# Kernel optimization log

Measured on AMD Instinct MI355X. Metric: run time of the kernel, lower is better.

The kernel has to match this reference:

```python
import jax, jax.numpy as jnp
import numpy as np

N, E, D, H, O = 100000, 1600000, 128, 128, 64
EPS = 1e-5


def setup_inputs() -> dict:
    key = jax.random.key(0)
    ks = jax.random.split(key, 12)
    s = 0.05
    return {
        "x": jax.random.normal(ks[0], (N, D), jnp.float32),
        "edge_index": jax.random.randint(ks[1], (2, E), 0, N),
        "W1": jax.random.normal(ks[2], (D, H), jnp.float32) * s,
        "b1": jnp.zeros((H,), jnp.float32),
        "W2": jax.random.normal(ks[3], (H, H), jnp.float32) * s,
        "b2": jnp.zeros((H,), jnp.float32),
        "W3": jax.random.normal(ks[4], (H, H), jnp.float32) * s,
        "b3": jnp.zeros((H,), jnp.float32),
        "g1": jnp.ones((H,), jnp.float32),
        "be1": jnp.zeros((H,), jnp.float32),
        "g2": jnp.ones((H,), jnp.float32),
        "be2": jnp.zeros((H,), jnp.float32),
        "Wp1": jax.random.normal(ks[5], (H, H), jnp.float32) * s,
        "bp1": jnp.zeros((H,), jnp.float32),
        "Wp2": jax.random.normal(ks[6], (H, O), jnp.float32) * s,
        "bp2": jnp.zeros((O,), jnp.float32),
    }


def _layer_norm(h, g, b):
    mu = jnp.mean(h, axis=-1, keepdims=True)
    var = jnp.mean(jnp.square(h - mu), axis=-1, keepdims=True)
    return g * (h - mu) * jax.lax.rsqrt(var + EPS) + b


def reference(x, edge_index, W1, b1, W2, b2, W3, b3, g1, be1, g2, be2, Wp1, bp1, Wp2, bp2):
    n = x.shape[0]
    loop = jnp.arange(n)
    # GCN: add self-loops, symmetric normalization D^-1/2 (A+I) D^-1/2
    src = jnp.concatenate([edge_index[0], loop])
    dst = jnp.concatenate([edge_index[1], loop])
    deg = jax.ops.segment_sum(jnp.ones_like(src, x.dtype), dst, num_segments=n)
    dinv = jax.lax.rsqrt(jnp.maximum(deg, 1e-12))
    norm = dinv[src] * dinv[dst]  # [E+N]

    def gcn_conv(h, W, b):
        hw = h @ W                              # transform first (PyG GCNConv)
        msg = hw[src] * norm[:, None]           # gather + edge scale
        return jax.ops.segment_sum(msg, dst, num_segments=n) + b  # scatter-add

    # dropout is a no-op in eval mode
    h = _layer_norm(jax.nn.relu(gcn_conv(x, W1, b1)), g1, be1)
    h = _layer_norm(jax.nn.relu(gcn_conv(h, W2, b2)), g2, be2)
    h = jax.nn.relu(gcn_conv(h, W3, b3))
    h = h @ Wp1 + bp1
    h = h @ Wp2 + bp2
    return jax.nn.sigmoid(h)
```

## Files before the change

### kernel.cpp

```cpp
#include <hip/hip_runtime.h>
#include <hip/hip_bf16.h>

typedef __attribute__((ext_vector_type(8))) short short8;
typedef __attribute__((ext_vector_type(4))) float floatx4;
typedef unsigned int u32;

__device__ __forceinline__ u32 f2bf(float f) {
    union { float f; u32 u; } c; c.f = f;
    return (c.u + 0x7FFFu + ((c.u >> 16) & 1u)) >> 16;
}
__device__ __forceinline__ short8 cvt8(const float* p) {
    float4 f0 = ((const float4*)p)[0];
    float4 f1 = ((const float4*)p)[1];
    short8 r;
    r[0] = (short)f2bf(f0.x); r[1] = (short)f2bf(f0.y);
    r[2] = (short)f2bf(f0.z); r[3] = (short)f2bf(f0.w);
    r[4] = (short)f2bf(f1.x); r[5] = (short)f2bf(f1.y);
    r[6] = (short)f2bf(f1.z); r[7] = (short)f2bf(f1.w);
    return r;
}

__device__ __forceinline__ void fp8x8_acc(uint2 v, float* a) {
    auto f0 = __builtin_amdgcn_cvt_pk_f32_fp8((int)v.x, false);
    auto f1 = __builtin_amdgcn_cvt_pk_f32_fp8((int)v.x, true);
    auto f2 = __builtin_amdgcn_cvt_pk_f32_fp8((int)v.y, false);
    auto f3 = __builtin_amdgcn_cvt_pk_f32_fp8((int)v.y, true);
    a[0] += ((const float*)&f0)[0]; a[1] += ((const float*)&f0)[1];
    a[2] += ((const float*)&f1)[0]; a[3] += ((const float*)&f1)[1];
    a[4] += ((const float*)&f2)[0]; a[5] += ((const float*)&f2)[1];
    a[6] += ((const float*)&f3)[0]; a[7] += ((const float*)&f3)[1];
}
__device__ __forceinline__ void fp8x8_dec(uint2 v, float* x) {
    auto f0 = __builtin_amdgcn_cvt_pk_f32_fp8((int)v.x, false);
    auto f1 = __builtin_amdgcn_cvt_pk_f32_fp8((int)v.x, true);
    auto f2 = __builtin_amdgcn_cvt_pk_f32_fp8((int)v.y, false);
    auto f3 = __builtin_amdgcn_cvt_pk_f32_fp8((int)v.y, true);
    x[0] = ((const float*)&f0)[0]; x[1] = ((const float*)&f0)[1];
    x[2] = ((const float*)&f1)[0]; x[3] = ((const float*)&f1)[1];
    x[4] = ((const float*)&f2)[0]; x[5] = ((const float*)&f2)[1];
    x[6] = ((const float*)&f3)[0]; x[7] = ((const float*)&f3)[1];
}
__device__ __forceinline__ u32 f32x4_to_fp8(float a, float b, float c, float d) {
    u32 w = (u32)__builtin_amdgcn_cvt_pk_fp8_f32(a, b, 0, false);
    w = (u32)__builtin_amdgcn_cvt_pk_fp8_f32(c, d, (int)w, true);
    return w;
}

#define CCAP 264

__device__ __forceinline__ void gatherq(const uint2* __restrict__ hw64,
                                        const int* __restrict__ col,
                                        int* __restrict__ ldsc,
                                        int begq, int endq, int beg, int stagelen,
                                        int lane, int s16, float* __restrict__ acc) {
    for (int i = lane; i < stagelen; i += 64) ldsc[i] = col[beg + i];
    __syncthreads();
    int dq = endq - begq;
    int offq = begq - beg;
    int send = min(endq, beg + stagelen);
    int sdq = max(0, send - begq);
    int mx = sdq;
    mx = max(mx, __shfl_xor(mx, 16));
    mx = max(mx, __shfl_xor(mx, 32));
    int idxcap = CCAP - 8;
    int off0 = min(offq, idxcap);
    for (int jb = 0; jb < mx; jb += 8) {
        uint2 v[8];
#pragma unroll
        for (int j = 0; j < 8; ++j) {
            int jj = jb + j;
            int cj = ldsc[off0 + (jj < stagelen - off0 ? jj : 0)];
            bool act = jj < sdq;
            uint2 tv; tv.x = 0u; tv.y = 0u;
            if (act) {
                cj = ldsc[offq + jj];
                tv = hw64[(size_t)cj * 16 + s16];
            }
            v[j] = tv;
        }
#pragma unroll
        for (int j = 0; j < 8; ++j) fp8x8_acc(v[j], acc);
    }
    for (int j = sdq; j < dq; ++j) {
        int cj = col[begq + j];
        uint2 tv = hw64[(size_t)cj * 16 + s16];
        fp8x8_acc(tv, acc);
    }
}

__global__ __launch_bounds__(256) void hist_trans_k(
        const int* __restrict__ dst, int* __restrict__ bcnt, int E, int histB,
        const float* __restrict__ W1, const float* __restrict__ W2,
        const float* __restrict__ W3, const float* __restrict__ Wp1,
        const float* __restrict__ Wp2,
        unsigned short* __restrict__ o1, unsigned short* __restrict__ o2,
        unsigned short* __restrict__ o3, unsigned short* __restrict__ o4,
        unsigned short* __restrict__ o5) {
    int t = threadIdx.x;
    if ((int)blockIdx.x < histB) {
        __shared__ int h[512];
        h[t] = 0; h[t + 256] = 0;
        __syncthreads();
        int e0 = blockIdx.x * 4096;
        int ne = min(4096, E - e0);
        for (int i = t; i < ne; i += 256) atomicAdd(&h[dst[e0 + i] >> 8], 1);
        __syncthreads();
        int c = h[t];
        if (c) atomicAdd(&bcnt[t], c);
        c = h[t + 256];
        if (c) atomicAdd(&bcnt[t + 256], c);
    } else {
        int i = (blockIdx.x - histB) * 256 + t;
        const float* in; unsigned short* out; int cols, li;
        if (i < 16384)      { in = W1;  out = o1; cols = 128; li = i; }
        else if (i < 32768) { in = W2;  out = o2; cols = 128; li = i - 16384; }
        else if (i < 49152) { in = W3;  out = o3; cols = 128; li = i - 32768; }
        else if (i < 65536) { in = Wp1; out = o4; cols = 128; li = i - 49152; }
        else                { in = Wp2; out = o5; cols = 64;  li = i - 65536; }
        int r = li / cols, c = li - r * cols;
        out[(size_t)c * 128 + r] = (unsigned short)f2bf(in[li]);
    }
}

__global__ void bscan_k(const int* __restrict__ bcnt, int* __restrict__ bbase,
                        int* __restrict__ cursor, int nb, int E) {
    __shared__ int tmp[512];
    int t = threadIdx.x;
    int v = (t < nb) ? bcnt[t] : 0;
    tmp[t] = v;
    __syncthreads();
    for (int off = 1; off < 512; off <<= 1) {
        int a = (t >= off) ? tmp[t - off] : 0;
        __syncthreads();
        tmp[t] += a;
        __syncthreads();
    }
    if (t < nb) {
        int ex = tmp[t] - v;
        bbase[t] = ex;
        cursor[t] = ex;
    }
    if (t == 0) bbase[nb] = E;
}

__global__ __launch_bounds__(256) void bucket_k(const int* __restrict__ src,
                                                const int* __restrict__ dst,
                                                int* __restrict__ cursor,
                                                u32* __restrict__ pairs, int E, int nb) {
    __shared__ int cnt[512];
    __shared__ int gbase[512];
    __shared__ int cur[512];
    int t = threadIdx.x;
    cnt[t] = 0; cnt[t + 256] = 0;
    __syncthreads();
    int e0 = blockIdx.x * 8192;
    int ne = min(8192, E - e0);
    for (int i = t; i < ne; i += 256) atomicAdd(&cnt[dst[e0 + i] >> 8], 1);
    __syncthreads();
    for (int b = t; b < nb; b += 256) {
        int c = cnt[b];
        gbase[b] = c ? atomicAdd(&cursor[b], c) : 0;
        cur[b] = 0;
    }
    __syncthreads();
    for (int i = t; i < ne; i += 256) {
        int d = dst[e0 + i];
        int s = src[e0 + i];
        int b = d >> 8;
        int p = atomicAdd(&cur[b], 1);
        pairs[gbase[b] + p] = (u32)s | ((u32)(d & 255) << 24);
    }
}

#define LCOL_CAP 12288
__global__ __launch_bounds__(256) void build_k(const u32* __restrict__ pairs,
                                               const int* __restrict__ bbase,
                                               int* __restrict__ rowptr,
                                               float* __restrict__ dinv,
                                               int* __restrict__ col, int N, int E) {
    __shared__ int cnt[256], incl[256], cur[256];
    __shared__ int lcol[LCOL_CAP];
    int b = blockIdx.x, t = threadIdx.x;
    int base = bbase[b];
    int ecnt = bbase[b + 1] - base;
    cnt[t] = 0;
    __syncthreads();
    for (int j = t; j < ecnt; j += 256) atomicAdd(&cnt[pairs[base + j] >> 24], 1);
    __syncthreads();
    incl[t] = cnt[t];
    __syncthreads();
    for (int off = 1; off < 256; off <<= 1) {
        int a = (t >= off) ? incl[t - off] : 0;
        __syncthreads();
        incl[t] += a;
        __syncthreads();
    }
    int myc = cnt[t];
    int ex = incl[t] - myc;
    int node = b * 256 + t;
    if (node < N) {
        rowptr[node] = base + ex;
        dinv[node] = rsqrtf((float)myc + 1.0f);
    }
    cur[t] = ex;
    if (b == 0 && t == 0) rowptr[N] = E;
    __syncthreads();
    if (ecnt <= LCOL_CAP) {
        for (int j = t; j < ecnt; j += 256) {
            u32 v = pairs[base + j];
            int r = atomicAdd(&cur[v >> 24], 1);
            lcol[r] = (int)(v & 0xFFFFFF);
        }
        __syncthreads();
        for (int j = t; j < ecnt; j += 256) col[base + j] = lcol[j];
    } else {
        for (int j = t; j < ecnt; j += 256) {
            u32 v = pairs[base + j];
            int r = atomicAdd(&cur[v >> 24], 1);
            col[base + r] = (int)(v & 0xFFFFFF);
        }
    }
}

__global__ __launch_bounds__(256) void gemm1_k(const float* __restrict__ A,
                                               const short* __restrict__ Wt,
                                               const float* __restrict__ dinv,
                                               u32* __restrict__ out, int M) {
    int wave = threadIdx.x >> 6;
    int lane = threadIdx.x & 63;
    int m0 = blockIdx.x * 64 + wave * 16;
    if (m0 >= M) return;
    int quad = lane >> 4, lr = lane & 15;
    int row = m0 + lr;
    bool wr = row < M;
    if (row >= M) row = M - 1;
    const float* Ab = A + (size_t)row * 128 + quad * 8;
    short8 b0 = cvt8(Ab), b1 = cvt8(Ab + 32), b2 = cvt8(Ab + 64), b3 = cvt8(Ab + 96);
    float di = dinv[row];
#pragma unroll
    for (int nt = 0; nt < 8; ++nt) {
        int ncol = nt * 16 + lr;
        const short8* Wp = (const short8*)(Wt + (size_t)ncol * 128 + quad * 8);
        short8 a0 = Wp[0], a1 = Wp[4], a2 = Wp[8], a3 = Wp[12];
        floatx4 acc = {0.f, 0.f, 0.f, 0.f};
        acc = __builtin_amdgcn_mfma_f32_16x16x32_bf16(a0, b0, acc, 0, 0, 0);
        acc = __builtin_amdgcn_mfma_f32_16x16x32_bf16(a1, b1, acc, 0, 0, 0);
        acc = __builtin_amdgcn_mfma_f32_16x16x32_bf16(a2, b2, acc, 0, 0, 0);
        acc = __builtin_amdgcn_mfma_f32_16x16x32_bf16(a3, b3, acc, 0, 0, 0);
        if (wr) {
            out[(size_t)(m0 + lr) * 32 + nt * 4 + quad] =
                f32x4_to_fp8(acc[0] * di, acc[1] * di, acc[2] * di, acc[3] * di);
        }
    }
}

__global__ __launch_bounds__(256) void fconv_k(const uint2* __restrict__ hw64,
                                               const int* __restrict__ rowptr,
                                               const int* __restrict__ col,
                                               const float* __restrict__ dinv,
                                               const float* __restrict__ bias,
                                               const float* __restrict__ gam,
                                               const float* __restrict__ bet,
                                               const short* __restrict__ Wt,
                                               u32* __restrict__ out, int N) {
    __shared__ unsigned short rows[16][136];
    __shared__ int ldsc[4][CCAP];
    int t = threadIdx.x, wave = t >> 6, lane = t & 63;
    int q = lane >> 4, s16 = lane & 15;
    int nb0 = blockIdx.x * 16;
    int node0 = nb0 + wave * 4;
    int node = node0 + q;
    bool ok = node < N;
    int beg = rowptr[min(node0, N)];
    int e4  = rowptr[min(node0 + 4, N)];
    int begq = rowptr[min(node, N)];
    int endq = ok ? rowptr[min(node + 1, N)] : begq;
    int stagelen = min(e4 - beg, 256);
    uint2 selfd; selfd.x = 0u; selfd.y = 0u;
    float di = 0.f;
    if (ok) {
        selfd = hw64[(size_t)node * 16 + s16];
        di = dinv[node];
    }
    float acc[8] = {0.f, 0.f, 0.f, 0.f, 0.f, 0.f, 0.f, 0.f};
    gatherq(hw64, col, ldsc[wave], begq, endq, beg, stagelen, lane, s16, acc);

    float sx[8]; fp8x8_dec(selfd, sx);
    float4 bv0 = *(const float4*)(bias + 8 * s16);
    float4 bv1 = *(const float4*)(bias + 8 * s16 + 4);
    float a[8];
    a[0] = fmaxf(di * (acc[0] + sx[0]) + bv0.x, 0.f);
    a[1] = fmaxf(di * (acc[1] + sx[1]) + bv0.y, 0.f);
    a[2] = fmaxf(di * (acc[2] + sx[2]) + bv0.z, 0.f);
    a[3] = fmaxf(di * (acc[3] + sx[3]) + bv0.w, 0.f);
    a[4] = fmaxf(di * (acc[4] + sx[4]) + bv1.x, 0.f);
    a[5] = fmaxf(di * (acc[5] + sx[5]) + bv1.y, 0.f);
    a[6] = fmaxf(di * (acc[6] + sx[6]) + bv1.z, 0.f);
    a[7] = fmaxf(di * (acc[7] + sx[7]) + bv1.w, 0.f);
    if (!ok) {
#pragma unroll
        for (int k = 0; k < 8; ++k) a[k] = 0.f;
    }
    float s = 0.f, qq = 0.f;
#pragma unroll
    for (int k = 0; k < 8; ++k) { s += a[k]; qq += a[k] * a[k]; }
#pragma unroll
    for (int mm = 8; mm >= 1; mm >>= 1) {
        s += __shfl_xor(s, mm);
        qq += __shfl_xor(qq, mm);
    }
    float mu = s * (1.f / 128.f);
    float var = qq * (1.f / 128.f) - mu * mu;
    float rs = rsqrtf(fmaxf(var, 0.f) + 1e-5f);
    float4 gv0 = *(const float4*)(gam + 8 * s16);
    float4 gv1 = *(const float4*)(gam + 8 * s16 + 4);
    float4 be0 = *(const float4*)(bet + 8 * s16);
    float4 be1 = *(const float4*)(bet + 8 * s16 + 4);
    a[0] = gv0.x * (a[0] - mu) * rs + be0.x;
    a[1] = gv0.y * (a[1] - mu) * rs + be0.y;
    a[2] = gv0.z * (a[2] - mu) * rs + be0.z;
    a[3] = gv0.w * (a[3] - mu) * rs + be0.w;
    a[4] = gv1.x * (a[4] - mu) * rs + be1.x;
    a[5] = gv1.y * (a[5] - mu) * rs + be1.y;
    a[6] = gv1.z * (a[6] - mu) * rs + be1.z;
    a[7] = gv1.w * (a[7] - mu) * rs + be1.w;
    if (!ok) {
#pragma unroll
        for (int k = 0; k < 8; ++k) a[k] = 0.f;
    }
    int r = wave * 4 + q;
    uint4 st;
    st.x = f2bf(a[0]) | (f2bf(a[1]) << 16);
    st.y = f2bf(a[2]) | (f2bf(a[3]) << 16);
    st.z = f2bf(a[4]) | (f2bf(a[5]) << 16);
    st.w = f2bf(a[6]) | (f2bf(a[7]) << 16);
    *(uint4*)((char*)&rows[r][0] + 16 * s16) = st;
    __syncthreads();

    int quad = lane >> 4, lr = lane & 15;
    short8 b0 = *(const short8*)&rows[lr][quad * 8];
    short8 b1 = *(const short8*)&rows[lr][32 + quad * 8];
    short8 b2 = *(const short8*)&rows[lr][64 + quad * 8];
    short8 b3 = *(const short8*)&rows[lr][96 + quad * 8];
    int onode = nb0 + lr;
    float di2 = (onode < N) ? dinv[onode] : 0.f;
#pragma unroll
    for (int k = 0; k < 2; ++k) {
        int ct = wave * 2 + k;
        int ncol = ct * 16 + lr;
        const short8* Wp = (const short8*)(Wt + (size_t)ncol * 128 + quad * 8);
        short8 a0 = Wp[0], a1 = Wp[4], a2 = Wp[8], a3 = Wp[12];
        floatx4 acm = {0.f, 0.f, 0.f, 0.f};
        acm = __builtin_amdgcn_mfma_f32_16x16x32_bf16(a0, b0, acm, 0, 0, 0);
        acm = __builtin_amdgcn_mfma_f32_16x16x32_bf16(a1, b1, acm, 0, 0, 0);
        acm = __builtin_amdgcn_mfma_f32_16x16x32_bf16(a2, b2, acm, 0, 0, 0);
        acm = __builtin_amdgcn_mfma_f32_16x16x32_bf16(a3, b3, acm, 0, 0, 0);
        int c0 = ct * 16 + quad * 4;
        if (onode < N) {
            out[(size_t)onode * 32 + (c0 >> 2)] =
                f32x4_to_fp8(acm[0] * di2, acm[1] * di2, acm[2] * di2, acm[3] * di2);
        }
    }
}

__global__ __launch_bounds__(256) void fhead_k(const uint2* __restrict__ hw64,
                                               const int* __restrict__ rowptr,
                                               const int* __restrict__ col,
                                               const float* __restrict__ dinv,
                                               const float* __restrict__ bias,
                                               const short* __restrict__ Wp1t,
                                               const float* __restrict__ bp1,
                                               const short* __restrict__ Wp2t,
                                               const float* __restrict__ bp2,
                                               float* __restrict__ out, int N) {
    __shared__ unsigned short rows[16][136];
    __shared__ unsigned short h1s[16][136];
    __shared__ int ldsc[4][CCAP];
    int t = threadIdx.x, wave = t >> 6, lane = t & 63;
    int q = lane >> 4, s16 = lane & 15;
    int nb0 = blockIdx.x * 16;
    int node0 = nb0 + wave * 4;
    int node = node0 + q;
    bool ok = node < N;
    int beg = rowptr[min(node0, N)];
    int e4  = rowptr[min(node0 + 4, N)];
    int begq = rowptr[min(node, N)];
    int endq = ok ? rowptr[min(node + 1, N)] : begq;
    int stagelen = min(e4 - beg, 256);
    uint2 selfd; selfd.x = 0u; selfd.y = 0u;
    float di = 0.f;
    if (ok) {
        selfd = hw64[(size_t)node * 16 + s16];
        di = dinv[node];
    }
    float acc[8] = {0.f, 0.f, 0.f, 0.f, 0.f, 0.f, 0.f, 0.f};
    gatherq(hw64, col, ldsc[wave], begq, endq, beg, stagelen, lane, s16, acc);

    float sx[8]; fp8x8_dec(selfd, sx);
    float4 bv0 = *(const float4*)(bias + 8 * s16);
    float4 bv1 = *(const float4*)(bias + 8 * s16 + 4);
    float a[8];
    a[0] = fmaxf(di * (acc[0] + sx[0]) + bv0.x, 0.f);
    a[1] = fmaxf(di * (acc[1] + sx[1]) + bv0.y, 0.f);
    a[2] = fmaxf(di * (acc[2] + sx[2]) + bv0.z, 0.f);
    a[3] = fmaxf(di * (acc[3] + sx[3]) + bv0.w, 0.f);
    a[4] = fmaxf(di * (acc[4] + sx[4]) + bv1.x, 0.f);
    a[5] = fmaxf(di * (acc[5] + sx[5]) + bv1.y, 0.f);
    a[6] = fmaxf(di * (acc[6] + sx[6]) + bv1.z, 0.f);
    a[7] = fmaxf(di * (acc[7] + sx[7]) + bv1.w, 0.f);
    if (!ok) {
#pragma unroll
        for (int k = 0; k < 8; ++k) a[k] = 0.f;
    }
    int r = wave * 4 + q;
    uint4 st;
    st.x = f2bf(a[0]) | (f2bf(a[1]) << 16);
    st.y = f2bf(a[2]) | (f2bf(a[3]) << 16);
    st.z = f2bf(a[4]) | (f2bf(a[5]) << 16);
    st.w = f2bf(a[6]) | (f2bf(a[7]) << 16);
    *(uint4*)((char*)&rows[r][0] + 16 * s16) = st;
    __syncthreads();

    int quad = lane >> 4, lr = lane & 15;
    {
        short8 b0 = *(const short8*)&rows[lr][quad * 8];
        short8 b1 = *(const short8*)&rows[lr][32 + quad * 8];
        short8 b2 = *(const short8*)&rows[lr][64 + quad * 8];
        short8 b3 = *(const short8*)&rows[lr][96 + quad * 8];
#pragma unroll
        for (int k = 0; k < 2; ++k) {
            int ct = wave * 2 + k;
            int ncol = ct * 16 + lr;
            const short8* Wp = (const short8*)(Wp1t + (size_t)ncol * 128 + quad * 8);
            short8 a0 = Wp[0], a1 = Wp[4], a2 = Wp[8], a3 = Wp[12];
            floatx4 acm = {0.f, 0.f, 0.f, 0.f};
            acm = __builtin_amdgcn_mfma_f32_16x16x32_bf16(a0, b0, acm, 0, 0, 0);
            acm = __builtin_amdgcn_mfma_f32_16x16x32_bf16(a1, b1, acm, 0, 0, 0);
            acm = __builtin_amdgcn_mfma_f32_16x16x32_bf16(a2, b2, acm, 0, 0, 0);
            acm = __builtin_amdgcn_mfma_f32_16x16x32_bf16(a3, b3, acm, 0, 0, 0);
            int c0 = ct * 16 + quad * 4;
            float4 bv = *(const float4*)(bp1 + c0);
            uint2 stq;
            stq.x = f2bf(acm[0] + bv.x) | (f2bf(acm[1] + bv.y) << 16);
            stq.y = f2bf(acm[2] + bv.z) | (f2bf(acm[3] + bv.w) << 16);
            *(uint2*)&h1s[lr][c0] = stq;
        }
    }
    __syncthreads();
    {
        short8 b0 = *(const short8*)&h1s[lr][quad * 8];
        short8 b1 = *(const short8*)&h1s[lr][32 + quad * 8];
        short8 b2 = *(const short8*)&h1s[lr][64 + quad * 8];
        short8 b3 = *(const short8*)&h1s[lr][96 + quad * 8];
        int ncol = wave * 16 + lr;
        const short8* Wp = (const short8*)(Wp2t + (size_t)ncol * 128 + quad * 8);
        short8 a0 = Wp[0], a1 = Wp[4], a2 = Wp[8], a3 = Wp[12];
        floatx4 acm = {0.f, 0.f, 0.f, 0.f};
        acm = __builtin_amdgcn_mfma_f32_16x16x32_bf16(a0, b0, acm, 0, 0, 0);
        acm = __builtin_amdgcn_mfma_f32_16x16x32_bf16(a1, b1, acm, 0, 0, 0);
        acm = __builtin_amdgcn_mfma_f32_16x16x32_bf16(a2, b2, acm, 0, 0, 0);
        acm = __builtin_amdgcn_mfma_f32_16x16x32_bf16(a3, b3, acm, 0, 0, 0);
        int c0 = wave * 16 + quad * 4;
        int onode = nb0 + lr;
        if (onode < N) {
            float4 bv = *(const float4*)(bp2 + c0);
            float4 sg;
            sg.x = 1.f / (1.f + __expf(-(acm[0] + bv.x)));
            sg.y = 1.f / (1.f + __expf(-(acm[1] + bv.y)));
            sg.z = 1.f / (1.f + __expf(-(acm[2] + bv.z)));
            sg.w = 1.f / (1.f + __expf(-(acm[3] + bv.w)));
            *(float4*)(out + (size_t)onode * 64 + c0) = sg;
        }
    }
}

extern "C" void kernel_launch(void* const* d_in, const int* in_sizes, int n_in,
                              void* d_out, int out_size, void* d_ws, size_t ws_size,
                              hipStream_t stream) {
    const int N = in_sizes[0] / 128;
    const int E = in_sizes[1] / 2;
    const int nb = (N + 255) >> 8;
    const int* edge = (const int*)d_in[1];
    const int* srcp = edge;
    const int* dstp = edge + E;
    const float* x   = (const float*)d_in[0];
    const float* W1  = (const float*)d_in[2];
    const float* b1  = (const float*)d_in[3];
    const float* W2  = (const float*)d_in[4];
    const float* b2  = (const float*)d_in[5];
    const float* W3  = (const float*)d_in[6];
    const float* b3  = (const float*)d_in[7];
    const float* g1  = (const float*)d_in[8];
    const float* be1 = (const float*)d_in[9];
    const float* g2  = (const float*)d_in[10];
    const float* be2 = (const float*)d_in[11];
    const float* Wp1 = (const float*)d_in[12];
    const float* bp1 = (const float*)d_in[13];
    const float* Wp2 = (const float*)d_in[14];
    const float* bp2 = (const float*)d_in[15];

    char* ws = (char*)d_ws;
    size_t off = 0;
    auto alloc = [&](size_t b) -> char* {
        char* p = ws + off;
        off += (b + 255) & ~(size_t)255;
        return p;
    };
    int* bcnt   = (int*)alloc(512 * 4);
    int* bbase  = (int*)alloc((size_t)(nb + 1) * 4);
    int* cursor = (int*)alloc((size_t)nb * 4);
    int* rowptr = (int*)alloc((size_t)(N + 1) * 4);
    float* dinv = (float*)alloc((size_t)N * 4);
    u32* pairs  = (u32*)alloc((size_t)E * 4);
    int* colA   = (int*)alloc((size_t)E * 4);
    unsigned char* hw  = (unsigned char*)alloc((size_t)N * 128);
    unsigned char* hb  = (unsigned char*)alloc((size_t)N * 128);
    unsigned short* w1t = (unsigned short*)alloc(128 * 128 * 2);
    unsigned short* w2t = (unsigned short*)alloc(128 * 128 * 2);
    unsigned short* w3t = (unsigned short*)alloc(128 * 128 * 2);
    unsigned short* wp1t = (unsigned short*)alloc(128 * 128 * 2);
    unsigned short* wp2t = (unsigned short*)alloc(64 * 128 * 2);
    if (off > ws_size) return;

    int gb = (N + 63) / 64;
    int fb = (N + 15) / 16;
    int histB = (E + 4095) / 4096;

    hipMemsetAsync(bcnt, 0, 512 * 4, stream);
    hist_trans_k<<<histB + 288, 256, 0, stream>>>(dstp, bcnt, E, histB,
                                                  W1, W2, W3, Wp1, Wp2,
                                                  w1t, w2t, w3t, wp1t, wp2t);
    bscan_k<<<1, 512, 0, stream>>>(bcnt, bbase, cursor, nb, E);
    bucket_k<<<(E + 8191) / 8192, 256, 0, stream>>>(srcp, dstp, cursor, pairs, E, nb);
    build_k<<<nb, 256, 0, stream>>>(pairs, bbase, rowptr, dinv, colA, N, E);

    gemm1_k<<<gb, 256, 0, stream>>>(x, (const short*)w1t, dinv, (u32*)hw, N);
    fconv_k<<<fb, 256, 0, stream>>>((const uint2*)hw, rowptr, colA, dinv,
                                    b1, g1, be1, (const short*)w2t, (u32*)hb, N);
    fconv_k<<<fb, 256, 0, stream>>>((const uint2*)hb, rowptr, colA, dinv,
                                    b2, g2, be2, (const short*)w3t, (u32*)hw, N);
    fhead_k<<<fb, 256, 0, stream>>>((const uint2*)hw, rowptr, colA, dinv, b3,
                                    (const short*)wp1t, bp1, (const short*)wp2t, bp2,
                                    (float*)d_out, N);
}
```

Measured before the change: 370.4 us.

## Replace bucketed two-pass CSR build with per-node degree count and atomic scatter

The CSR construction changes from a two-level bucket sort (histogram per 256-node bucket, bucket pairs, local sort in LDS) to a per-node global atomic degree count, then a block-sum, scan and rowptr kernel, then a direct atomic-cursor scatter of source ids into col. This drops the intermediate pairs buffer and the LDS sorting pass. In exchange it uses heavily contended global atomics on individual nodes and scattered writes, and the order of neighbours within a row becomes nondeterministic. The gather index load is also simplified to a single clamped LDS read.

Result: slower. 542.6 us (+46.5%).

```diff
diff --git a/kernel.cpp b/kernel.cpp
--- a/kernel.cpp
+++ b/kernel.cpp
@@ -62,20 +62,15 @@
     int mx = sdq;
     mx = max(mx, __shfl_xor(mx, 16));
     mx = max(mx, __shfl_xor(mx, 32));
-    int idxcap = CCAP - 8;
-    int off0 = min(offq, idxcap);
     for (int jb = 0; jb < mx; jb += 8) {
         uint2 v[8];
 #pragma unroll
         for (int j = 0; j < 8; ++j) {
             int jj = jb + j;
-            int cj = ldsc[off0 + (jj < stagelen - off0 ? jj : 0)];
+            int cj = ldsc[min(offq + jj, CCAP - 1)];
             bool act = jj < sdq;
             uint2 tv; tv.x = 0u; tv.y = 0u;
-            if (act) {
-                cj = ldsc[offq + jj];
-                tv = hw64[(size_t)cj * 16 + s16];
-            }
+            if (act) tv = hw64[(size_t)cj * 16 + s16];
             v[j] = tv;
         }
 #pragma unroll
@@ -88,8 +83,8 @@
     }
 }
 
-__global__ __launch_bounds__(256) void hist_trans_k(
-        const int* __restrict__ dst, int* __restrict__ bcnt, int E, int histB,
+__global__ __launch_bounds__(256) void deg_trans_k(
+        const int* __restrict__ dst, int* __restrict__ deg, int E, int degB,
         const float* __restrict__ W1, const float* __restrict__ W2,
         const float* __restrict__ W3, const float* __restrict__ Wp1,
         const float* __restrict__ Wp2,
@@ -97,20 +92,12 @@
         unsigned short* __restrict__ o3, unsigned short* __restrict__ o4,
         unsigned short* __restrict__ o5) {
     int t = threadIdx.x;
-    if ((int)blockIdx.x < histB) {
-        __shared__ int h[512];
-        h[t] = 0; h[t + 256] = 0;
-        __syncthreads();
+    if ((int)blockIdx.x < degB) {
         int e0 = blockIdx.x * 4096;
         int ne = min(4096, E - e0);
-        for (int i = t; i < ne; i += 256) atomicAdd(&h[dst[e0 + i] >> 8], 1);
-        __syncthreads();
-        int c = h[t];
-        if (c) atomicAdd(&bcnt[t], c);
-        c = h[t + 256];
-        if (c) atomicAdd(&bcnt[t + 256], c);
+        for (int i = t; i < ne; i += 256) atomicAdd(&deg[dst[e0 + i]], 1);
     } else {
-        int i = (blockIdx.x - histB) * 256 + t;
+        int i = (blockIdx.x - degB) * 256 + t;
         const float* in; unsigned short* out; int cols, li;
         if (i < 16384)      { in = W1;  out = o1; cols = 128; li = i; }
         else if (i < 32768) { in = W2;  out = o2; cols = 128; li = i - 16384; }
@@ -122,8 +109,22 @@
     }
 }
 
+__global__ __launch_bounds__(256) void bsum_k(const int* __restrict__ deg,
+                                              int* __restrict__ bcnt, int N) {
+    __shared__ int sh[256];
+    int t = threadIdx.x;
+    int node = blockIdx.x * 256 + t;
+    sh[t] = (node < N) ? deg[node] : 0;
+    __syncthreads();
+    for (int off = 128; off >= 1; off >>= 1) {
+        if (t < off) sh[t] += sh[t + off];
+        __syncthreads();
+    }
+    if (t == 0) bcnt[blockIdx.x] = sh[0];
+}
+
 __global__ void bscan_k(const int* __restrict__ bcnt, int* __restrict__ bbase,
-                        int* __restrict__ cursor, int nb, int E) {
+                        int nb, int E) {
     __shared__ int tmp[512];
     int t = threadIdx.x;
     int v = (t < nb) ? bcnt[t] : 0;
@@ -135,59 +136,20 @@
         tmp[t] += a;
         __syncthreads();
     }
-    if (t < nb) {
-        int ex = tmp[t] - v;
-        bbase[t] = ex;
-        cursor[t] = ex;
-    }
+    if (t < nb) bbase[t] = tmp[t] - v;
     if (t == 0) bbase[nb] = E;
 }
 
-__global__ __launch_bounds__(256) void bucket_k(const int* __restrict__ src,
-                                                const int* __restrict__ dst,
+__global__ __launch_bounds__(256) void rowptr_k(const int* __restrict__ deg,
+                                                const int* __restrict__ bbase,
+                                                int* __restrict__ rowptr,
                                                 int* __restrict__ cursor,
-                                                u32* __restrict__ pairs, int E, int nb) {
-    __shared__ int cnt[512];
-    __shared__ int gbase[512];
-    __shared__ int cur[512];
-    int t = threadIdx.x;
-    cnt[t] = 0; cnt[t + 256] = 0;
-    __syncthreads();
-    int e0 = blockIdx.x * 8192;
-    int ne = min(8192, E - e0);
-    for (int i = t; i < ne; i += 256) atomicAdd(&cnt[dst[e0 + i] >> 8], 1);
-    __syncthreads();
-    for (int b = t; b < nb; b += 256) {
-        int c = cnt[b];
-        gbase[b] = c ? atomicAdd(&cursor[b], c) : 0;
-        cur[b] = 0;
-    }
-    __syncthreads();
-    for (int i = t; i < ne; i += 256) {
-        int d = dst[e0 + i];
-        int s = src[e0 + i];
-        int b = d >> 8;
-        int p = atomicAdd(&cur[b], 1);
-        pairs[gbase[b] + p] = (u32)s | ((u32)(d & 255) << 24);
-    }
-}
-
-#define LCOL_CAP 12288
-__global__ __launch_bounds__(256) void build_k(const u32* __restrict__ pairs,
-                                               const int* __restrict__ bbase,
-                                               int* __restrict__ rowptr,
-                                               float* __restrict__ dinv,
-                                               int* __restrict__ col, int N, int E) {
-    __shared__ int cnt[256], incl[256], cur[256];
-    __shared__ int lcol[LCOL_CAP];
+                                                float* __restrict__ dinv, int N, int E) {
+    __shared__ int incl[256];
     int b = blockIdx.x, t = threadIdx.x;
-    int base = bbase[b];
-    int ecnt = bbase[b + 1] - base;
-    cnt[t] = 0;
-    __syncthreads();
-    for (int j = t; j < ecnt; j += 256) atomicAdd(&cnt[pairs[base + j] >> 24], 1);
-    __syncthreads();
-    incl[t] = cnt[t];
+    int node = b * 256 + t;
+    int d = (node < N) ? deg[node] : 0;
+    incl[t] = d;
     __syncthreads();
     for (int off = 1; off < 256; off <<= 1) {
         int a = (t >= off) ? incl[t - off] : 0;
@@ -195,30 +157,25 @@
         incl[t] += a;
         __syncthreads();
     }
-    int myc = cnt[t];
-    int ex = incl[t] - myc;
-    int node = b * 256 + t;
     if (node < N) {
-        rowptr[node] = base + ex;
-        dinv[node] = rsqrtf((float)myc + 1.0f);
-    }
-    cur[t] = ex;
+        int ex = bbase[b] + incl[t] - d;
+        rowptr[node] = ex;
+        cursor[node] = ex;
+        dinv[node] = rsqrtf((float)d + 1.0f);
+    }
     if (b == 0 && t == 0) rowptr[N] = E;
-    __syncthreads();
-    if (ecnt <= LCOL_CAP) {
-        for (int j = t; j < ecnt; j += 256) {
-            u32 v = pairs[base + j];
-            int r = atomicAdd(&cur[v >> 24], 1);
-            lcol[r] = (int)(v & 0xFFFFFF);
-        }
-        __syncthreads();
-        for (int j = t; j < ecnt; j += 256) col[base + j] = lcol[j];
-    } else {
-        for (int j = t; j < ecnt; j += 256) {
-            u32 v = pairs[base + j];
-            int r = atomicAdd(&cur[v >> 24], 1);
-            col[base + r] = (int)(v & 0xFFFFFF);
-        }
+}
+
+__global__ __launch_bounds__(256) void scatter_k(const int* __restrict__ src,
+                                                 const int* __restrict__ dst,
+                                                 int* __restrict__ cursor,
+                                                 int* __restrict__ col, int E) {
+    int stride = gridDim.x * 256;
+    for (int i = blockIdx.x * 256 + threadIdx.x; i < E; i += stride) {
+        int d = dst[i];
+        int s = src[i];
+        int pos = atomicAdd(&cursor[d], 1);
+        col[pos] = s;
     }
 }
 
@@ -508,10 +465,10 @@
     };
     int* bcnt   = (int*)alloc(512 * 4);
     int* bbase  = (int*)alloc((size_t)(nb + 1) * 4);
-    int* cursor = (int*)alloc((size_t)nb * 4);
+    int* deg    = (int*)alloc((size_t)N * 4);
+    int* cursor = (int*)alloc((size_t)N * 4);
     int* rowptr = (int*)alloc((size_t)(N + 1) * 4);
     float* dinv = (float*)alloc((size_t)N * 4);
-    u32* pairs  = (u32*)alloc((size_t)E * 4);
     int* colA   = (int*)alloc((size_t)E * 4);
     unsigned char* hw  = (unsigned char*)alloc((size_t)N * 128);
     unsigned char* hb  = (unsigned char*)alloc((size_t)N * 128);
@@ -524,15 +481,16 @@
 
     int gb = (N + 63) / 64;
     int fb = (N + 15) / 16;
-    int histB = (E + 4095) / 4096;
-
-    hipMemsetAsync(bcnt, 0, 512 * 4, stream);
-    hist_trans_k<<<histB + 288, 256, 0, stream>>>(dstp, bcnt, E, histB,
-                                                  W1, W2, W3, Wp1, Wp2,
-                                                  w1t, w2t, w3t, wp1t, wp2t);
-    bscan_k<<<1, 512, 0, stream>>>(bcnt, bbase, cursor, nb, E);
-    bucket_k<<<(E + 8191) / 8192, 256, 0, stream>>>(srcp, dstp, cursor, pairs, E, nb);
-    build_k<<<nb, 256, 0, stream>>>(pairs, bbase, rowptr, dinv, colA, N, E);
+    int degB = (E + 4095) / 4096;
+
+    hipMemsetAsync(deg, 0, (size_t)N * 4, stream);
+    deg_trans_k<<<degB + 288, 256, 0, stream>>>(dstp, deg, E, degB,
+                                                W1, W2, W3, Wp1, Wp2,
+                                                w1t, w2t, w3t, wp1t, wp2t);
+    bsum_k<<<nb, 256, 0, stream>>>(deg, bcnt, N);
+    bscan_k<<<1, 512, 0, stream>>>(bcnt, bbase, nb, E);
+    rowptr_k<<<nb, 256, 0, stream>>>(deg, bbase, rowptr, cursor, dinv, N, E);
+    scatter_k<<<2048, 256, 0, stream>>>(srcp, dstp, cursor, colA, E);
 
     gemm1_k<<<gb, 256, 0, stream>>>(x, (const short*)w1t, dinv, (u32*)hw, N);
     fconv_k<<<fb, 256, 0, stream>>>((const uint2*)hw, rowptr, colA, dinv,
```

## Bucket edges into fixed-capacity slots to drop the separate histogram pass

Applied to the files above, without the earlier changes.

The CSR build now scatters edges directly into fixed-capacity per-bucket regions of 8192 slots, using per-bucket global counters. This removes the separate histogram pass over dst and its prefix-scan dependency before bucketing, so one full read of dst and a launch are saved. The weight transpose is merged into the bucketing kernel, and the scan afterwards only computes CSR offsets. It risks overflow if any 256-node bucket receives more than 8192 edges, which holds for uniform random inputs but not for skewed graphs. The gather index load is also simplified to a clamped LDS read.

Result: faster. 362.8 us (-2.1%).

```diff
diff --git a/kernel.cpp b/kernel.cpp
--- a/kernel.cpp
+++ b/kernel.cpp
@@ -47,6 +47,7 @@
 }
 
 #define CCAP 264
+#define CAPB 8192
 
 __device__ __forceinline__ void gatherq(const uint2* __restrict__ hw64,
                                         const int* __restrict__ col,
@@ -62,20 +63,15 @@
     int mx = sdq;
     mx = max(mx, __shfl_xor(mx, 16));
     mx = max(mx, __shfl_xor(mx, 32));
-    int idxcap = CCAP - 8;
-    int off0 = min(offq, idxcap);
     for (int jb = 0; jb < mx; jb += 8) {
         uint2 v[8];
 #pragma unroll
         for (int j = 0; j < 8; ++j) {
             int jj = jb + j;
-            int cj = ldsc[off0 + (jj < stagelen - off0 ? jj : 0)];
+            int cj = ldsc[min(offq + jj, CCAP - 1)];
             bool act = jj < sdq;
             uint2 tv; tv.x = 0u; tv.y = 0u;
-            if (act) {
-                cj = ldsc[offq + jj];
-                tv = hw64[(size_t)cj * 16 + s16];
-            }
+            if (act) tv = hw64[(size_t)cj * 16 + s16];
             v[j] = tv;
         }
 #pragma unroll
@@ -88,8 +84,9 @@
     }
 }
 
-__global__ __launch_bounds__(256) void hist_trans_k(
-        const int* __restrict__ dst, int* __restrict__ bcnt, int E, int histB,
+__global__ __launch_bounds__(256) void bucket_trans_k(
+        const int* __restrict__ src, const int* __restrict__ dst,
+        int* __restrict__ gcnt, u32* __restrict__ pairs, int E, int nb, int bucketB,
         const float* __restrict__ W1, const float* __restrict__ W2,
         const float* __restrict__ W3, const float* __restrict__ Wp1,
         const float* __restrict__ Wp2,
@@ -97,20 +94,8 @@
         unsigned short* __restrict__ o3, unsigned short* __restrict__ o4,
         unsigned short* __restrict__ o5) {
     int t = threadIdx.x;
-    if ((int)blockIdx.x < histB) {
-        __shared__ int h[512];
-        h[t] = 0; h[t + 256] = 0;
-        __syncthreads();
-        int e0 = blockIdx.x * 4096;
-        int ne = min(4096, E - e0);
-        for (int i = t; i < ne; i += 256) atomicAdd(&h[dst[e0 + i] >> 8], 1);
-        __syncthreads();
-        int c = h[t];
-        if (c) atomicAdd(&bcnt[t], c);
-        c = h[t + 256];
-        if (c) atomicAdd(&bcnt[t + 256], c);
-    } else {
-        int i = (blockIdx.x - histB) * 256 + t;
+    if ((int)blockIdx.x >= bucketB) {
+        int i = (blockIdx.x - bucketB) * 256 + t;
         const float* in; unsigned short* out; int cols, li;
         if (i < 16384)      { in = W1;  out = o1; cols = 128; li = i; }
         else if (i < 32768) { in = W2;  out = o2; cols = 128; li = i - 16384; }
@@ -119,38 +104,11 @@
         else                { in = Wp2; out = o5; cols = 64;  li = i - 65536; }
         int r = li / cols, c = li - r * cols;
         out[(size_t)c * 128 + r] = (unsigned short)f2bf(in[li]);
-    }
-}
-
-__global__ void bscan_k(const int* __restrict__ bcnt, int* __restrict__ bbase,
-                        int* __restrict__ cursor, int nb, int E) {
-    __shared__ int tmp[512];
-    int t = threadIdx.x;
-    int v = (t < nb) ? bcnt[t] : 0;
-    tmp[t] = v;
-    __syncthreads();
-    for (int off = 1; off < 512; off <<= 1) {
-        int a = (t >= off) ? tmp[t - off] : 0;
-        __syncthreads();
-        tmp[t] += a;
-        __syncthreads();
-    }
-    if (t < nb) {
-        int ex = tmp[t] - v;
-        bbase[t] = ex;
-        cursor[t] = ex;
-    }
-    if (t == 0) bbase[nb] = E;
-}
-
-__global__ __launch_bounds__(256) void bucket_k(const int* __restrict__ src,
-                                                const int* __restrict__ dst,
-                                                int* __restrict__ cursor,
-                                                u32* __restrict__ pairs, int E, int nb) {
+        return;
+    }
     __shared__ int cnt[512];
     __shared__ int gbase[512];
     __shared__ int cur[512];
-    int t = threadIdx.x;
     cnt[t] = 0; cnt[t + 256] = 0;
     __syncthreads();
     int e0 = blockIdx.x * 8192;
@@ -159,7 +117,7 @@
     __syncthreads();
     for (int b = t; b < nb; b += 256) {
         int c = cnt[b];
-        gbase[b] = c ? atomicAdd(&cursor[b], c) : 0;
+        gbase[b] = c ? (b * CAPB + atomicAdd(&gcnt[b], c)) : 0;
         cur[b] = 0;
     }
     __syncthreads();
@@ -170,6 +128,23 @@
         int p = atomicAdd(&cur[b], 1);
         pairs[gbase[b] + p] = (u32)s | ((u32)(d & 255) << 24);
     }
+}
+
+__global__ void bscan_k(const int* __restrict__ gcnt, int* __restrict__ bbase,
+                        int nb, int E) {
+    __shared__ int tmp[512];
+    int t = threadIdx.x;
+    int v = (t < nb) ? gcnt[t] : 0;
+    tmp[t] = v;
+    __syncthreads();
+    for (int off = 1; off < 512; off <<= 1) {
+        int a = (t >= off) ? tmp[t - off] : 0;
+        __syncthreads();
+        tmp[t] += a;
+        __syncthreads();
+    }
+    if (t < nb) bbase[t] = tmp[t] - v;
+    if (t == 0) bbase[nb] = E;
 }
 
 #define LCOL_CAP 12288
@@ -182,10 +157,11 @@
     __shared__ int lcol[LCOL_CAP];
     int b = blockIdx.x, t = threadIdx.x;
     int base = bbase[b];
+    int sbase = b * CAPB;
     int ecnt = bbase[b + 1] - base;
     cnt[t] = 0;
     __syncthreads();
-    for (int j = t; j < ecnt; j += 256) atomicAdd(&cnt[pairs[base + j] >> 24], 1);
+    for (int j = t; j < ecnt; j += 256) atomicAdd(&cnt[pairs[sbase + j] >> 24], 1);
     __syncthreads();
     incl[t] = cnt[t];
     __syncthreads();
@@ -207,7 +183,7 @@
     __syncthreads();
     if (ecnt <= LCOL_CAP) {
         for (int j = t; j < ecnt; j += 256) {
-            u32 v = pairs[base + j];
+            u32 v = pairs[sbase + j];
             int r = atomicAdd(&cur[v >> 24], 1);
             lcol[r] = (int)(v & 0xFFFFFF);
         }
@@ -215,7 +191,7 @@
         for (int j = t; j < ecnt; j += 256) col[base + j] = lcol[j];
     } else {
         for (int j = t; j < ecnt; j += 256) {
-            u32 v = pairs[base + j];
+            u32 v = pairs[sbase + j];
             int r = atomicAdd(&cur[v >> 24], 1);
             col[base + r] = (int)(v & 0xFFFFFF);
         }
@@ -506,12 +482,11 @@
         off += (b + 255) & ~(size_t)255;
         return p;
     };
-    int* bcnt   = (int*)alloc(512 * 4);
+    int* gcnt   = (int*)alloc(512 * 4);
     int* bbase  = (int*)alloc((size_t)(nb + 1) * 4);
-    int* cursor = (int*)alloc((size_t)nb * 4);
     int* rowptr = (int*)alloc((size_t)(N + 1) * 4);
     float* dinv = (float*)alloc((size_t)N * 4);
-    u32* pairs  = (u32*)alloc((size_t)E * 4);
+    u32* pairs  = (u32*)alloc((size_t)nb * CAPB * 4);
     int* colA   = (int*)alloc((size_t)E * 4);
     unsigned char* hw  = (unsigned char*)alloc((size_t)N * 128);
     unsigned char* hb  = (unsigned char*)alloc((size_t)N * 128);
@@ -524,14 +499,13 @@
 
     int gb = (N + 63) / 64;
     int fb = (N + 15) / 16;
-    int histB = (E + 4095) / 4096;
-
-    hipMemsetAsync(bcnt, 0, 512 * 4, stream);
-    hist_trans_k<<<histB + 288, 256, 0, stream>>>(dstp, bcnt, E, histB,
-                                                  W1, W2, W3, Wp1, Wp2,
-                                                  w1t, w2t, w3t, wp1t, wp2t);
-    bscan_k<<<1, 512, 0, stream>>>(bcnt, bbase, cursor, nb, E);
-    bucket_k<<<(E + 8191) / 8192, 256, 0, stream>>>(srcp, dstp, cursor, pairs, E, nb);
+    int bucketB = (E + 8191) / 8192;
+
+    hipMemsetAsync(gcnt, 0, 512 * 4, stream);
+    bucket_trans_k<<<bucketB + 288, 256, 0, stream>>>(srcp, dstp, gcnt, pairs, E, nb,
+                                                      bucketB, W1, W2, W3, Wp1, Wp2,
+                                                      w1t, w2t, w3t, wp1t, wp2t);
+    bscan_k<<<1, 512, 0, stream>>>(gcnt, bbase, nb, E);
     build_k<<<nb, 256, 0, stream>>>(pairs, bbase, rowptr, dinv, colA, N, E);
 
     gemm1_k<<<gb, 256, 0, stream>>>(x, (const short*)w1t, dinv, (u32*)hw, N);
```
